# Optimization experiments

Hardware: AMD Instinct MI355X
Metric: run time of the kernel (lower is better)

The kernel has to match this reference:

```python
import jax, jax.numpy as jnp
from jax import lax
import numpy as np

EPS = 4e-3            # geoopt float32 ball boundary eps
MAXNORM = 1.0 - EPS   # c = 1 Poincare ball


def _norm(x):
    return jnp.sqrt(jnp.maximum(jnp.sum(x * x, axis=-1, keepdims=True), 1e-15))


def expmap0(u):
    n = _norm(u)
    return jnp.tanh(n) * u / n


def projx(x):
    n = _norm(x)
    return jnp.where(n > MAXNORM, x * (MAXNORM / n), x)


def mobius_add(x, y):
    x2 = jnp.sum(x * x, -1, keepdims=True)
    y2 = jnp.sum(y * y, -1, keepdims=True)
    xy = jnp.sum(x * y, -1, keepdims=True)
    num = (1.0 + 2.0 * xy + y2) * x + (1.0 - x2) * y
    den = 1.0 + 2.0 * xy + x2 * y2
    return num / jnp.maximum(den, 1e-15)


def mamba_layer(x, inW, convW, convb, xpW, dtW, dtb, A_log, Dp, outW):
    # x: [B,T,H]; inW: [2*Din,H]; convW: [Din,K]; xpW: [R+2N,Din]; dtW: [Din,R]
    B, T, H = x.shape
    Din, N = A_log.shape
    K = convW.shape[-1]
    R = dtW.shape[-1]
    xz = jnp.einsum('bth,dh->btd', x, inW)              # [B,T,2*Din]
    xr, z = jnp.split(xz, 2, axis=-1)
    xc = lax.conv_general_dilated(jnp.transpose(xr, (0, 2, 1)), convW[:, None, :],
                                  (1,), [(K - 1, 0)], feature_group_count=Din)
    u = jax.nn.silu(jnp.transpose(xc + convb[None, :, None], (0, 2, 1)))  # [B,T,Din]
    x_dbl = jnp.einsum('btd,ed->bte', u, xpW)           # [B,T,R+2N]
    dt_r, Bm, Cm = x_dbl[..., :R], x_dbl[..., R:R + N], x_dbl[..., R + N:]
    dt = jax.nn.softplus(jnp.einsum('btr,dr->btd', dt_r, dtW) + dtb)      # [B,T,Din]
    A = -jnp.exp(A_log)                                 # [Din,N]
    dA = jnp.exp(dt[..., None] * A)                     # [B,T,Din,N]
    dBu = dt[..., None] * Bm[:, :, None, :] * u[..., None]

    def step(h, ins):
        dA_t, dBu_t, C_t = ins
        h = dA_t * h + dBu_t                            # [B,Din,N]
        return h, jnp.einsum('bdn,bn->bd', h, C_t)

    h0 = jnp.zeros((B, Din, N), x.dtype)
    _, ys = lax.scan(step, h0, (jnp.moveaxis(dA, 1, 0), jnp.moveaxis(dBu, 1, 0), jnp.moveaxis(Cm, 1, 0)))
    y = jnp.moveaxis(ys, 0, 1) + Dp * u                 # [B,T,Din]
    return jnp.einsum('btd,hd->bth', y * jax.nn.silu(z), outW)


def _encode(xs, inp_W, inp_b, in_proj_W, conv_W, conv_b, xproj_W, dt_W, dt_b, A_log, D_skip, out_W, outp_W, outp_b):
    # xs: [4,B,T,1]; params carry leading branch dim 4, then layer dim 3
    def branch(x, iW, ib, ipW, cW, cb, xpW, dW, db, Al, Dp, oW, opW, opb):
        h = jnp.einsum('bti,hi->bth', x, iW) + ib
        for l in range(ipW.shape[0]):
            h = mamba_layer(h, ipW[l], cW[l], cb[l], xpW[l], dW[l], db[l], Al[l], Dp[l], oW[l])
        return jnp.tanh(jnp.einsum('bth,eh->bte', h, opW) + opb)
    return jax.vmap(branch)(xs, inp_W, inp_b, in_proj_W, conv_W, conv_b, xproj_W, dt_W, dt_b, A_log, D_skip, out_W, outp_W, outp_b)


def setup_inputs() -> dict:
    key = jax.random.key(0)
    ks = jax.random.split(key, 24)
    Br, B, T, H, Din, N, K, R, E, L = 4, 32, 1024, 64, 128, 16, 4, 4, 32, 3

    def rn(k, shape, s=0.05):
        return jax.random.normal(k, shape, jnp.float32) * s

    A_init = jnp.log(jnp.arange(1, N + 1, dtype=jnp.float32))
    return {
        'trend': jax.random.normal(ks[0], (B, T, 1), jnp.float32),
        'seasonal_weekly': jax.random.normal(ks[1], (B, T, 1), jnp.float32),
        'seasonal_daily': jax.random.normal(ks[2], (B, T, 1), jnp.float32),
        'residual': jax.random.normal(ks[3], (B, T, 1), jnp.float32),
        'inp_W': rn(ks[4], (Br, H, 1), 0.5),
        'inp_b': rn(ks[5], (Br, H)),
        'in_proj_W': rn(ks[6], (Br, L, 2 * Din, H)),
        'conv_W': rn(ks[7], (Br, L, Din, K), 0.2),
        'conv_b': rn(ks[8], (Br, L, Din)),
        'xproj_W': rn(ks[9], (Br, L, R + 2 * N, Din)),
        'dt_W': rn(ks[10], (Br, L, Din, R), 0.2),
        'dt_b': rn(ks[11], (Br, L, Din), 0.5) - 4.0,  # softplus(dt_b) small
        'A_log': jnp.tile(A_init, (Br, L, Din, 1)) + rn(ks[12], (Br, L, Din, N), 0.01),
        'D_skip': jnp.ones((Br, L, Din), jnp.float32) + rn(ks[13], (Br, L, Din), 0.01),
        'out_W': rn(ks[14], (Br, L, H, Din)),
        'outp_W': rn(ks[15], (Br, E, H)),
        'outp_b': rn(ks[16], (Br, E)),
    }


def reference(trend, seasonal_weekly, seasonal_daily, residual, inp_W, inp_b, in_proj_W, conv_W, conv_b, xproj_W, dt_W, dt_b, A_log, D_skip, out_W, outp_W, outp_b):
    xs = jnp.stack([trend, seasonal_weekly, seasonal_daily, residual], 0)  # [4,B,T,1]
    z = _encode(xs, inp_W, inp_b, in_proj_W, conv_W, conv_b, xproj_W, dt_W, dt_b, A_log, D_skip, out_W, outp_W, outp_b)  # [4,B,T,E]
    zh = projx(expmap0(z))
    t, w, d, r = zh[0], zh[1], zh[2], zh[3]
    comb = projx(mobius_add(mobius_add(t, mobius_add(w, d)), r))
    # stacked [trend_h, weekly_h, daily_h, residual_h, combined_h]
    return jnp.stack([t, w, d, r, comb], 0)
```

## Files before the change

kernel.cpp:

```cpp
#include <hip/hip_runtime.h>
#include <math.h>

#define TT 1024
#define DIN 128
#define HH 64
#define NN 16
#define EE 32
#define LL 3
#define BB 32

__device__ __forceinline__ float siluf(float x) { return x / (1.f + __expf(-x)); }

typedef __attribute__((ext_vector_type(8))) short bf16x8;
typedef __attribute__((ext_vector_type(4))) float f32x4;

__device__ __forceinline__ void split2(float x, ushort& hi, ushort& lo) {
  unsigned u = __float_as_uint(x);
  hi = (ushort)(u >> 16);
  float rem = x - __uint_as_float((u >> 16) << 16);
  lo = (ushort)(__float_as_uint(rem) >> 16);
}

#define WXZ_N 196608
#define WXD_N 73728
#define WOUT_N 98304

__global__ __launch_bounds__(256) void k_presplit(
    const float* __restrict__ iprojW, const float* __restrict__ xprojW,
    const float* __restrict__ outW,
    ushort* __restrict__ WxzH, ushort* __restrict__ WxzL,
    ushort* __restrict__ WxdH, ushort* __restrict__ WxdL,
    ushort* __restrict__ WoH, ushort* __restrict__ WoL) {
  int idx = blockIdx.x * 256 + threadIdx.x;
  if (idx < WXZ_N) {
    ushort h, l;
    split2(iprojW[idx], h, l);
    WxzH[idx] = h; WxzL[idx] = l;
  }
  if (idx < WXD_N) {
    int k = idx & 127, r = (idx >> 7) % 48, bl = idx / (48 * 128);
    float v = (r < 36) ? xprojW[((size_t)(bl * 36 + r)) * 128 + k] : 0.f;
    ushort h, l;
    split2(v, h, l);
    WxdH[idx] = h; WxdL[idx] = l;
  }
  if (idx < WOUT_N) {
    ushort h, l;
    split2(outW[idx], h, l);
    WoH[idx] = h; WoL[idx] = l;
  }
}

__global__ __launch_bounds__(256) void k_xz(
    const float* __restrict__ x0, const float* __restrict__ x1,
    const float* __restrict__ x2, const float* __restrict__ x3,
    const float* __restrict__ h, const ushort* __restrict__ WH,
    const ushort* __restrict__ WL,
    const float* __restrict__ inpW, const float* __restrict__ inpb,
    float* __restrict__ xr, float* __restrict__ zb, int br0, int l) {
  __shared__ __align__(16) ushort Hh[64][72], Hl[64][72];
  const int tid = threadIdx.x;
  const int b  = blockIdx.y;
  const int t0 = blockIdx.x * 64;
  const int br = br0 + (b >> 5);
  const float* Hg = h + ((size_t)b * TT + t0) * HH;
  {
    const int row = tid >> 2, c0 = (tid & 3) * 16;
    float xv = 0.f;
    if (l == 0) {
      int bb = b & 31;
      const float* xp = (br == 0) ? x0 : (br == 1) ? x1 : (br == 2) ? x2 : x3;
      xv = xp[bb * TT + t0 + row];
    }
    #pragma unroll
    for (int q = 0; q < 4; ++q) {
      float4 hv;
      if (l == 0) {
        float4 w4 = *(const float4*)(inpW + br * HH + c0 + q * 4);
        float4 b4 = *(const float4*)(inpb + br * HH + c0 + q * 4);
        hv.x = xv * w4.x + b4.x; hv.y = xv * w4.y + b4.y;
        hv.z = xv * w4.z + b4.z; hv.w = xv * w4.w + b4.w;
      } else {
        hv = *(const float4*)(Hg + (size_t)row * HH + c0 + q * 4);
      }
      ushort h0,h1,h2,h3,l0,l1,l2,l3;
      split2(hv.x,h0,l0); split2(hv.y,h1,l1); split2(hv.z,h2,l2); split2(hv.w,h3,l3);
      *(ushort4*)&Hh[row][c0 + q*4] = make_ushort4(h0,h1,h2,h3);
      *(ushort4*)&Hl[row][c0 + q*4] = make_ushort4(l0,l1,l2,l3);
    }
  }
  __syncthreads();
  const int wave = tid >> 6, lane = tid & 63;
  const int quad = lane >> 4, l16 = lane & 15;
  const int nsub = (wave & 1) * 32, tsub = (wave >> 1) * 32;
  const size_t wbase = (size_t)(br * LL + l) * 256;
  for (int n0 = 0; n0 < 2 * DIN; n0 += 64) {
    f32x4 acc[2][2] = {};
    #pragma unroll
    for (int k0 = 0; k0 < 64; k0 += 32) {
      bf16x8 Ah[2], Al[2], Bh[2], Bl[2];
      #pragma unroll
      for (int i = 0; i < 2; ++i) {
        size_t ro = (wbase + n0 + nsub + i * 16 + l16) * 64 + k0 + quad * 8;
        Ah[i] = *(const bf16x8*)(WH + ro);
        Al[i] = *(const bf16x8*)(WL + ro);
        Bh[i] = *(const bf16x8*)&Hh[tsub + i*16 + l16][k0 + quad*8];
        Bl[i] = *(const bf16x8*)&Hl[tsub + i*16 + l16][k0 + quad*8];
      }
      #pragma unroll
      for (int i = 0; i < 2; ++i)
        #pragma unroll
        for (int j = 0; j < 2; ++j) {
          acc[i][j] = __builtin_amdgcn_mfma_f32_16x16x32_bf16(Ah[i], Bh[j], acc[i][j], 0, 0, 0);
          acc[i][j] = __builtin_amdgcn_mfma_f32_16x16x32_bf16(Ah[i], Bl[j], acc[i][j], 0, 0, 0);
          acc[i][j] = __builtin_amdgcn_mfma_f32_16x16x32_bf16(Al[i], Bh[j], acc[i][j], 0, 0, 0);
        }
    }
    #pragma unroll
    for (int i = 0; i < 2; ++i) {
      #pragma unroll
      for (int r = 0; r < 4; ++r) {
        int n = n0 + nsub + i*16 + quad*4 + r;
        float* dst = (n < DIN) ? (xr + ((size_t)b * DIN + n) * TT)
                               : (zb + ((size_t)b * DIN + (n - DIN)) * TT);
        #pragma unroll
        for (int j = 0; j < 2; ++j)
          dst[t0 + tsub + j*16 + l16] = acc[i][j][r];
      }
    }
  }
}

__global__ __launch_bounds__(256) void k_xds(
    const float* __restrict__ xr, const float* __restrict__ convW,
    const float* __restrict__ convb, const ushort* __restrict__ WH,
    const ushort* __restrict__ WL, const float* __restrict__ dtW,
    const float* __restrict__ dtb, const float* __restrict__ A_log,
    const float* __restrict__ D_skip,
    float* __restrict__ cd, float* __restrict__ Cm,
    float* __restrict__ Hloc, float* __restrict__ g, float* __restrict__ sdt,
    int br0, int l) {
  __shared__ __align__(16) float U[128][66];
  __shared__ __align__(16) float Xs[40][68];
  const int tid = threadIdx.x;
  const int b  = blockIdx.y;
  const int c  = blockIdx.x;
  const int t0 = c * 64;
  const int br = br0 + (b >> 5);
  const int wave = tid >> 6, lane = tid & 63;
  const int quad = lane >> 4, l16 = lane & 15;
  const int tw = wave * 16;
  const size_t wb48 = (size_t)(br * LL + l) * 48 * 128;
  const int dd = tid >> 1, p = tid & 1;
  {
    const int tb = t0 + p * 32;
    const float* src = xr + ((size_t)b * DIN + dd) * TT + tb;
    float r[36];
    #pragma unroll
    for (int q = 0; q < 9; ++q) {
      float4 f = make_float4(0.f, 0.f, 0.f, 0.f);
      if (q > 0 || tb > 0) f = *(const float4*)(src - 4 + q * 4);
      r[q*4+0] = f.x; r[q*4+1] = f.y; r[q*4+2] = f.z; r[q*4+3] = f.w;
    }
    const int wb0 = (br * LL + l) * DIN + dd;
    const float* w = convW + (size_t)wb0 * 4;
    const float w0 = w[0], w1 = w[1], w2 = w[2], w3 = w[3];
    const float cb = convb[wb0];
    #pragma unroll
    for (int i = 0; i < 32; i += 2) {
      float o0 = siluf(r[i+1]*w0 + r[i+2]*w1 + r[i+3]*w2 + r[i+4]*w3 + cb);
      float o1 = siluf(r[i+2]*w0 + r[i+3]*w1 + r[i+4]*w2 + r[i+5]*w3 + cb);
      *(float2*)&U[dd][p * 32 + i] = make_float2(o0, o1);
    }
  }
  __syncthreads();
  f32x4 acc[3] = {};
  #pragma unroll
  for (int k0 = 0; k0 < DIN; k0 += 32) {
    ushort bh[8], bl[8];
    #pragma unroll
    for (int j = 0; j < 8; ++j)
      split2(U[k0 + quad * 8 + j][tw + l16], bh[j], bl[j]);
    bf16x8 Bh = *(bf16x8*)bh, Bl = *(bf16x8*)bl;
    #pragma unroll
    for (int nf = 0; nf < 3; ++nf) {
      size_t ro = wb48 + (size_t)(nf * 16 + l16) * 128 + k0 + quad * 8;
      bf16x8 Whf = *(const bf16x8*)(WH + ro);
      bf16x8 Wlf = *(const bf16x8*)(WL + ro);
      acc[nf] = __builtin_amdgcn_mfma_f32_16x16x32_bf16(Whf, Bh, acc[nf], 0, 0, 0);
      acc[nf] = __builtin_amdgcn_mfma_f32_16x16x32_bf16(Whf, Bl, acc[nf], 0, 0, 0);
      acc[nf] = __builtin_amdgcn_mfma_f32_16x16x32_bf16(Wlf, Bh, acc[nf], 0, 0, 0);
    }
  }
  #pragma unroll
  for (int nf = 0; nf < 3; ++nf) {
    #pragma unroll
    for (int r = 0; r < 4; ++r) {
      int n = nf * 16 + quad * 4 + r;
      if (n < 40) Xs[n][tw + l16] = acc[nf][r];
    }
  }
  __syncthreads();
  {
    int n = tid >> 4, i0 = (tid & 15) * 4;
    *(float4*)(Cm + ((size_t)b * NN + n) * TT + t0 + i0) = *(float4*)&Xs[20 + n][i0];
  }
  const int n0s = p * 8;
  const int wbase = (br * LL + l) * DIN + dd;
  const float* wd = dtW + (size_t)wbase * 4;
  const float w0 = wd[0], w1 = wd[1], w2 = wd[2], w3 = wd[3];
  const float bias = dtb[wbase];
  float Ac[8];
  #pragma unroll
  for (int j = 0; j < 8; ++j) Ac[j] = -__expf(A_log[(size_t)wbase * NN + n0s + j]);
  const float Dp = D_skip[wbase];
  float hst[8] = {0.f,0.f,0.f,0.f,0.f,0.f,0.f,0.f};
  float sd = 0.f;
  float* gp  = g  + ((size_t)b * DIN + dd) * TT + t0;
  float* cdp = cd + ((size_t)b * DIN + dd) * TT + t0;
  for (int t8 = 0; t8 < 64; t8 += 8) {
    float4 a0 = *(const float4*)&Xs[0][t8], a0b = *(const float4*)&Xs[0][t8 + 4];
    float4 a1 = *(const float4*)&Xs[1][t8], a1b = *(const float4*)&Xs[1][t8 + 4];
    float4 a2 = *(const float4*)&Xs[2][t8], a2b = *(const float4*)&Xs[2][t8 + 4];
    float4 a3 = *(const float4*)&Xs[3][t8], a3b = *(const float4*)&Xs[3][t8 + 4];
    float x0v[8] = {a0.x,a0.y,a0.z,a0.w,a0b.x,a0b.y,a0b.z,a0b.w};
    float x1v[8] = {a1.x,a1.y,a1.z,a1.w,a1b.x,a1b.y,a1b.z,a1b.w};
    float x2v[8] = {a2.x,a2.y,a2.z,a2.w,a2b.x,a2b.y,a2b.z,a2b.w};
    float x3v[8] = {a3.x,a3.y,a3.z,a3.w,a3b.x,a3b.y,a3b.z,a3b.w};
    float us[8];
    {
      float2 u0 = *(const float2*)&U[dd][t8];
      float2 u1 = *(const float2*)&U[dd][t8 + 2];
      float2 u2 = *(const float2*)&U[dd][t8 + 4];
      float2 u3 = *(const float2*)&U[dd][t8 + 6];
      us[0]=u0.x; us[1]=u0.y; us[2]=u1.x; us[3]=u1.y;
      us[4]=u2.x; us[5]=u2.y; us[6]=u3.x; us[7]=u3.y;
    }
    float dts[8], cds[8], du[8];
    #pragma unroll
    for (int s = 0; s < 8; ++s) {
      float sv = x0v[s]*w0 + x1v[s]*w1 + x2v[s]*w2 + x3v[s]*w3 + bias;
      float e = __expf(-fabsf(sv));
      float dtv = fmaxf(sv, 0.f) + __logf(1.f + e);
      sd += dtv;
      dts[s] = dtv;
      cds[s] = sd;
      du[s] = dtv * us[s];
    }
    float acc8[8] = {0.f,0.f,0.f,0.f,0.f,0.f,0.f,0.f};
    #pragma unroll
    for (int j = 0; j < 8; ++j) {
      int n = n0s + j;
      float4 bq0 = *(const float4*)&Xs[4 + n][t8];
      float4 bq1 = *(const float4*)&Xs[4 + n][t8 + 4];
      float4 cq0 = *(const float4*)&Xs[20 + n][t8];
      float4 cq1 = *(const float4*)&Xs[20 + n][t8 + 4];
      float Bv[8] = {bq0.x,bq0.y,bq0.z,bq0.w,bq1.x,bq1.y,bq1.z,bq1.w};
      float Cv[8] = {cq0.x,cq0.y,cq0.z,cq0.w,cq1.x,cq1.y,cq1.z,cq1.w};
      float hj = hst[j], an = Ac[j];
      #pragma unroll
      for (int s = 0; s < 8; ++s) {
        hj = __expf(dts[s] * an) * hj + du[s] * Bv[s];
        acc8[s] += hj * Cv[s];
      }
      hst[j] = hj;
    }
    #pragma unroll
    for (int s = 0; s < 8; ++s) {
      float tot = acc8[s] + __shfl_xor(acc8[s], 1, 2);
      acc8[s] = tot + Dp * us[s];
    }
    if (p == 0) {
      *(float4*)(gp + t8)      = make_float4(acc8[0], acc8[1], acc8[2], acc8[3]);
      *(float4*)(gp + t8 + 4)  = make_float4(acc8[4], acc8[5], acc8[6], acc8[7]);
      *(float4*)(cdp + t8)     = make_float4(cds[0], cds[1], cds[2], cds[3]);
      *(float4*)(cdp + t8 + 4) = make_float4(cds[4], cds[5], cds[6], cds[7]);
    }
  }
  {
    float* hp = Hloc + (((size_t)b * DIN + dd) * 16 + c) * 16 + n0s;
    *(float4*)hp       = make_float4(hst[0], hst[1], hst[2], hst[3]);
    *(float4*)(hp + 4) = make_float4(hst[4], hst[5], hst[6], hst[7]);
  }
  if (p == 0) sdt[((size_t)b * DIN + dd) * 16 + c] = sd;
}

__global__ __launch_bounds__(256) void k_scan2(
    const float* __restrict__ cdc, const float* __restrict__ Cm,
    const float* __restrict__ A_log, const float* __restrict__ Hloc,
    const float* __restrict__ sdt, float* __restrict__ g, int br0, int l) {
  __shared__ __align__(16) float Cl[16][68];
  __shared__ __align__(16) float HinL[32][16];
  const int bx  = blockIdx.x;
  const int b   = bx / 60;
  const int rem = bx % 60;
  const int c   = (rem >> 2) + 1;
  const int dq  = rem & 3;
  const int tid = threadIdx.x;
  const int br  = br0 + (b >> 5);
  {
    int row = tid >> 4, cc = (tid & 15) * 4;
    *(float4*)&Cl[row][cc] = *(const float4*)(Cm + ((size_t)b * NN + row) * TT + c * 64 + cc);
  }
  const int dloc = tid >> 3, tg = tid & 7;
  const int d  = dq * 32 + dloc;
  size_t off = ((size_t)b * DIN + d) * TT + c * 64 + tg * 8;
  float* gp = g + off;
  float4 y0 = *(const float4*)gp;
  float4 y1 = *(const float4*)(gp + 4);
  float4 cq0 = *(const float4*)(cdc + off);
  float4 cq1 = *(const float4*)(cdc + off + 4);
  {
    int n0 = (tid & 7) * 2;
    int wbase = (br * LL + l) * DIN + d;
    float a0 = -__expf(A_log[(size_t)wbase * NN + n0]);
    float a1 = -__expf(A_log[(size_t)wbase * NN + n0 + 1]);
    float h0 = 0.f, h1 = 0.f;
    const float* sp  = sdt + ((size_t)b * DIN + d) * 16;
    const float* hlb = Hloc + ((size_t)b * DIN + d) * 256;
    for (int cc = 0; cc < c; ++cc) {
      float sdv = sp[cc];
      float2 hl = *(const float2*)(hlb + cc * 16 + n0);
      h0 = __expf(a0 * sdv) * h0 + hl.x;
      h1 = __expf(a1 * sdv) * h1 + hl.y;
    }
    HinL[dloc][n0] = h0;
    HinL[dloc][n0 + 1] = h1;
  }
  __syncthreads();
  float cd8[8] = {cq0.x, cq0.y, cq0.z, cq0.w, cq1.x, cq1.y, cq1.z, cq1.w};
  const float* al = A_log + (size_t)((br * LL + l) * DIN + d) * NN;
  float Ac16[16];
  #pragma unroll
  for (int n = 0; n < 16; ++n) Ac16[n] = -__expf(al[n]);
  float y8[8] = {y0.x, y0.y, y0.z, y0.w, y1.x, y1.y, y1.z, y1.w};
  const int tbase = tg * 8;
  #pragma unroll
  for (int n = 0; n < 16; ++n) {
    float hv = HinL[dloc][n];
    float an = Ac16[n];
    #pragma unroll
    for (int s = 0; s < 8; ++s)
      y8[s] += Cl[n][tbase + s] * __expf(an * cd8[s]) * hv;
  }
  *(float4*)gp       = make_float4(y8[0], y8[1], y8[2], y8[3]);
  *(float4*)(gp + 4) = make_float4(y8[4], y8[5], y8[6], y8[7]);
}

__global__ __launch_bounds__(256) void k_outxz(
    const float* __restrict__ graw, float* zb,
    const ushort* __restrict__ WoHp, const ushort* __restrict__ WoLp,
    const ushort* __restrict__ WxHp, const ushort* __restrict__ WxLp,
    float* __restrict__ xr, int br0, int l) {
  __shared__ __align__(16) ushort Bh_[64][72], Bl_[64][72];
  const int tid = threadIdx.x;
  const int b  = blockIdx.y;
  const int t0 = blockIdx.x * 64;
  const int br = br0 + (b >> 5);
  const int wave = tid >> 6, lane = tid & 63;
  const int quad = lane >> 4, l16 = lane & 15;
  const int hsub = (wave & 1) * 32, tsub = (wave >> 1) * 32;
  const size_t wbo = (size_t)(br * LL + l) * 64;
  f32x4 acc[2][2] = {};
  for (int k0 = 0; k0 < DIN; k0 += 64) {
    __syncthreads();
    {
      int row = tid >> 2, c0 = (tid & 3) * 16;
      #pragma unroll
      for (int q = 0; q < 4; ++q) {
        size_t off = ((size_t)b * DIN + k0 + row) * TT + t0 + c0 + q * 4;
        float4 gv = *(const float4*)(graw + off);
        float4 zv = *(const float4*)(zb + off);
        float a0 = gv.x * siluf(zv.x), a1 = gv.y * siluf(zv.y);
        float a2 = gv.z * siluf(zv.z), a3 = gv.w * siluf(zv.w);
        ushort h0,h1,h2,h3,l0,l1,l2,l3;
        split2(a0,h0,l0); split2(a1,h1,l1); split2(a2,h2,l2); split2(a3,h3,l3);
        *(ushort4*)&Bh_[row][c0 + q*4] = make_ushort4(h0,h1,h2,h3);
        *(ushort4*)&Bl_[row][c0 + q*4] = make_ushort4(l0,l1,l2,l3);
      }
    }
    __syncthreads();
    #pragma unroll
    for (int kk = 0; kk < 64; kk += 32) {
      bf16x8 Ahf[2], Alf[2], Bhf[2], Blf[2];
      #pragma unroll
      for (int i = 0; i < 2; ++i) {
        size_t ro = (wbo + hsub + i * 16 + l16) * 128 + k0 + kk + quad * 8;
        Ahf[i] = *(const bf16x8*)(WoHp + ro);
        Alf[i] = *(const bf16x8*)(WoLp + ro);
        Bhf[i] = *(const bf16x8*)&Bh_[tsub + i*16 + l16][kk + quad*8];
        Blf[i] = *(const bf16x8*)&Bl_[tsub + i*16 + l16][kk + quad*8];
      }
      #pragma unroll
      for (int i = 0; i < 2; ++i)
        #pragma unroll
        for (int j = 0; j < 2; ++j) {
          acc[i][j] = __builtin_amdgcn_mfma_f32_16x16x32_bf16(Ahf[i], Bhf[j], acc[i][j], 0, 0, 0);
          acc[i][j] = __builtin_amdgcn_mfma_f32_16x16x32_bf16(Ahf[i], Blf[j], acc[i][j], 0, 0, 0);
          acc[i][j] = __builtin_amdgcn_mfma_f32_16x16x32_bf16(Alf[i], Bhf[j], acc[i][j], 0, 0, 0);
        }
    }
  }
  __syncthreads();
  #pragma unroll
  for (int i = 0; i < 2; ++i) {
    int hh0 = hsub + i*16 + quad*4;
    #pragma unroll
    for (int j = 0; j < 2; ++j) {
      int t = tsub + j*16 + l16;
      ushort h0,h1,h2,h3,l0,l1,l2,l3;
      split2(acc[i][j][0],h0,l0); split2(acc[i][j][1],h1,l1);
      split2(acc[i][j][2],h2,l2); split2(acc[i][j][3],h3,l3);
      *(ushort2*)&Bh_[t][hh0]     = make_ushort2(h0,h1);
      *(ushort2*)&Bh_[t][hh0 + 2] = make_ushort2(h2,h3);
      *(ushort2*)&Bl_[t][hh0]     = make_ushort2(l0,l1);
      *(ushort2*)&Bl_[t][hh0 + 2] = make_ushort2(l2,l3);
    }
  }
  __syncthreads();
  const size_t wbase = (size_t)(br * LL + (l + 1)) * 256;
  const int nsub = hsub;
  for (int n0 = 0; n0 < 2 * DIN; n0 += 64) {
    f32x4 a2[2][2] = {};
    #pragma unroll
    for (int k0 = 0; k0 < 64; k0 += 32) {
      bf16x8 Ah[2], Al[2], Bh[2], Bl[2];
      #pragma unroll
      for (int i = 0; i < 2; ++i) {
        size_t ro = (wbase + n0 + nsub + i * 16 + l16) * 64 + k0 + quad * 8;
        Ah[i] = *(const bf16x8*)(WxHp + ro);
        Al[i] = *(const bf16x8*)(WxLp + ro);
        Bh[i] = *(const bf16x8*)&Bh_[tsub + i*16 + l16][k0 + quad*8];
        Bl[i] = *(const bf16x8*)&Bl_[tsub + i*16 + l16][k0 + quad*8];
      }
      #pragma unroll
      for (int i = 0; i < 2; ++i)
        #pragma unroll
        for (int j = 0; j < 2; ++j) {
          a2[i][j] = __builtin_amdgcn_mfma_f32_16x16x32_bf16(Ah[i], Bh[j], a2[i][j], 0, 0, 0);
          a2[i][j] = __builtin_amdgcn_mfma_f32_16x16x32_bf16(Ah[i], Bl[j], a2[i][j], 0, 0, 0);
          a2[i][j] = __builtin_amdgcn_mfma_f32_16x16x32_bf16(Al[i], Bh[j], a2[i][j], 0, 0, 0);
        }
    }
    #pragma unroll
    for (int i = 0; i < 2; ++i) {
      #pragma unroll
      for (int r = 0; r < 4; ++r) {
        int n = n0 + nsub + i*16 + quad*4 + r;
        float* dst = (n < DIN) ? (xr + ((size_t)b * DIN + n) * TT)
                               : (zb + ((size_t)b * DIN + (n - DIN)) * TT);
        #pragma unroll
        for (int j = 0; j < 2; ++j)
          dst[t0 + tsub + j*16 + l16] = a2[i][j][r];
      }
    }
  }
}

__global__ __launch_bounds__(256) void k_out(
    const float* __restrict__ graw, const float* __restrict__ zb,
    const ushort* __restrict__ WH, const ushort* __restrict__ WL,
    float* __restrict__ h, int br0, int l) {
  __shared__ __align__(16) ushort Bh_[64][72], Bl_[64][72];
  const int tid = threadIdx.x;
  const int b  = blockIdx.y;
  const int t0 = blockIdx.x * 64;
  const int br = br0 + (b >> 5);
  const int wave = tid >> 6, lane = tid & 63;
  const int quad = lane >> 4, l16 = lane & 15;
  const int hsub = (wave & 1) * 32, tsub = (wave >> 1) * 32;
  const size_t wb = (size_t)(br * LL + l) * 64;
  f32x4 acc[2][2] = {};
  for (int k0 = 0; k0 < DIN; k0 += 64) {
    __syncthreads();
    {
      int row = tid >> 2, c0 = (tid & 3) * 16;
      #pragma unroll
      for (int q = 0; q < 4; ++q) {
        size_t off = ((size_t)b * DIN + k0 + row) * TT + t0 + c0 + q * 4;
        float4 gv = *(const float4*)(graw + off);
        float4 zv = *(const float4*)(zb + off);
        float a0 = gv.x * siluf(zv.x), a1 = gv.y * siluf(zv.y);
        float a2 = gv.z * siluf(zv.z), a3 = gv.w * siluf(zv.w);
        ushort h0,h1,h2,h3,l0,l1,l2,l3;
        split2(a0,h0,l0); split2(a1,h1,l1); split2(a2,h2,l2); split2(a3,h3,l3);
        *(ushort4*)&Bh_[row][c0 + q*4] = make_ushort4(h0,h1,h2,h3);
        *(ushort4*)&Bl_[row][c0 + q*4] = make_ushort4(l0,l1,l2,l3);
      }
    }
    __syncthreads();
    #pragma unroll
    for (int kk = 0; kk < 64; kk += 32) {
      bf16x8 Ahf[2], Alf[2], Bhf[2], Blf[2];
      #pragma unroll
      for (int i = 0; i < 2; ++i) {
        size_t ro = (wb + hsub + i * 16 + l16) * 128 + k0 + kk + quad * 8;
        Ahf[i] = *(const bf16x8*)(WH + ro);
        Alf[i] = *(const bf16x8*)(WL + ro);
        Bhf[i] = *(const bf16x8*)&Bh_[tsub + i*16 + l16][kk + quad*8];
        Blf[i] = *(const bf16x8*)&Bl_[tsub + i*16 + l16][kk + quad*8];
      }
      #pragma unroll
      for (int i = 0; i < 2; ++i)
        #pragma unroll
        for (int j = 0; j < 2; ++j) {
          acc[i][j] = __builtin_amdgcn_mfma_f32_16x16x32_bf16(Ahf[i], Bhf[j], acc[i][j], 0, 0, 0);
          acc[i][j] = __builtin_amdgcn_mfma_f32_16x16x32_bf16(Ahf[i], Blf[j], acc[i][j], 0, 0, 0);
          acc[i][j] = __builtin_amdgcn_mfma_f32_16x16x32_bf16(Alf[i], Bhf[j], acc[i][j], 0, 0, 0);
        }
    }
  }
  #pragma unroll
  for (int i = 0; i < 2; ++i) {
    int hh0 = hsub + i*16 + quad*4;
    #pragma unroll
    for (int j = 0; j < 2; ++j) {
      int t = t0 + tsub + j*16 + l16;
      *(f32x4*)(h + ((size_t)b * TT + t) * HH + hh0) = acc[i][j];
    }
  }
}

__global__ __launch_bounds__(256) void k_ze(
    const float* __restrict__ h, const float* __restrict__ outpW,
    const float* __restrict__ outpb, float* __restrict__ ze, int br0) {
  __shared__ __align__(16) float As[16][132];
  __shared__ __align__(16) float Ws[16][36];
  __shared__ __align__(16) float Cs[128][36];
  const int tid = threadIdx.x;
  const int b  = blockIdx.y;
  const int t0 = blockIdx.x * 128;
  const int br = br0 + (b >> 5);
  const float* W = outpW + (size_t)br * EE * HH;
  float acc[4][4] = {};
  const int ti = tid & 31, ni = tid >> 5;
  for (int k0 = 0; k0 < HH; k0 += 16) {
    __syncthreads();
    {
      int i = tid >> 1, kq = (tid & 1) * 8;
      const float* src = h + ((size_t)b * TT + t0 + i) * HH + k0 + kq;
      float4 a0 = *(const float4*)src;
      float4 a1 = *(const float4*)(src + 4);
      As[kq+0][i]=a0.x; As[kq+1][i]=a0.y; As[kq+2][i]=a0.z; As[kq+3][i]=a0.w;
      As[kq+4][i]=a1.x; As[kq+5][i]=a1.y; As[kq+6][i]=a1.z; As[kq+7][i]=a1.w;
    }
    for (int idx = tid; idx < 512; idx += 256) {
      int jj = idx >> 4, kk = idx & 15;
      Ws[kk][jj] = W[(size_t)jj * HH + k0 + kk];
    }
    __syncthreads();
    #pragma unroll
    for (int kk = 0; kk < 16; ++kk) {
      float4 a = *(const float4*)&As[kk][ti * 4];
      float4 w = *(const float4*)&Ws[kk][ni * 4];
      acc[0][0] += a.x*w.x; acc[0][1] += a.x*w.y; acc[0][2] += a.x*w.z; acc[0][3] += a.x*w.w;
      acc[1][0] += a.y*w.x; acc[1][1] += a.y*w.y; acc[1][2] += a.y*w.z; acc[1][3] += a.y*w.w;
      acc[2][0] += a.z*w.x; acc[2][1] += a.z*w.y; acc[2][2] += a.z*w.z; acc[2][3] += a.z*w.w;
      acc[3][0] += a.w*w.x; acc[3][1] += a.w*w.y; acc[3][2] += a.w*w.z; acc[3][3] += a.w*w.w;
    }
  }
  __syncthreads();
  float bj[4];
  #pragma unroll
  for (int c = 0; c < 4; ++c) bj[c] = outpb[br * EE + ni*4 + c];
  #pragma unroll
  for (int r = 0; r < 4; ++r)
    #pragma unroll
    for (int c = 0; c < 4; ++c)
      Cs[ti*4+r][ni*4+c] = tanhf(acc[r][c] + bj[c]);
  __syncthreads();
  int i = tid >> 1, j16 = (tid & 1) * 16;
  float* dst = ze + (((size_t)(br0 * 32 + b)) * TT + t0 + i) * EE + j16;
  #pragma unroll
  for (int q = 0; q < 4; ++q)
    *(float4*)(dst + q*4) = *(float4*)&Cs[i][j16 + q*4];
}

__device__ __forceinline__ void mobius_add32(const float* x, const float* y, float* o) {
  float x2 = 0.f, y2 = 0.f, xy = 0.f;
  #pragma unroll
  for (int i = 0; i < 32; ++i) { x2 += x[i]*x[i]; y2 += y[i]*y[i]; xy += x[i]*y[i]; }
  float ca  = 1.f + 2.f*xy + y2;
  float cb  = 1.f - x2;
  float den = 1.f + 2.f*xy + x2*y2;
  float inv = 1.f / fmaxf(den, 1e-15f);
  #pragma unroll
  for (int i = 0; i < 32; ++i) o[i] = (ca*x[i] + cb*y[i]) * inv;
}

__global__ __launch_bounds__(256) void k_hyper(const float* __restrict__ ze,
                                               float* __restrict__ out) {
  int idx = blockIdx.x * 256 + threadIdx.x;
  int b = idx >> 10, t = idx & 1023;
  float v[4][32];
  #pragma unroll
  for (int br = 0; br < 4; ++br) {
    const float* p = ze + (((size_t)br * BB + b) * TT + t) * EE;
    float s = 0.f;
    #pragma unroll
    for (int e = 0; e < 32; ++e) { v[br][e] = p[e]; s += v[br][e]*v[br][e]; }
    float nr = sqrtf(fmaxf(s, 1e-15f));
    float sc = tanhf(nr) / nr;
    float s2 = 0.f;
    #pragma unroll
    for (int e = 0; e < 32; ++e) { v[br][e] *= sc; s2 += v[br][e]*v[br][e]; }
    float n2 = sqrtf(fmaxf(s2, 1e-15f));
    if (n2 > 0.996f) {
      float sc2 = 0.996f / n2;
      #pragma unroll
      for (int e = 0; e < 32; ++e) v[br][e] *= sc2;
    }
    float* o = out + (((size_t)br * BB + b) * TT + t) * EE;
    #pragma unroll
    for (int e = 0; e < 32; ++e) o[e] = v[br][e];
  }
  float m1[32], m2[32];
  mobius_add32(v[1], v[2], m1);
  mobius_add32(v[0], m1, m2);
  mobius_add32(m2, v[3], m1);
  float s = 0.f;
  #pragma unroll
  for (int e = 0; e < 32; ++e) s += m1[e]*m1[e];
  float n = sqrtf(fmaxf(s, 1e-15f));
  if (n > 0.996f) {
    float sc = 0.996f / n;
    #pragma unroll
    for (int e = 0; e < 32; ++e) m1[e] *= sc;
  }
  float* o = out + (((size_t)4 * BB + b) * TT + t) * EE;
  #pragma unroll
  for (int e = 0; e < 32; ++e) o[e] = m1[e];
}

extern "C" void kernel_launch(void* const* d_in, const int* in_sizes, int n_in,
                              void* d_out, int out_size, void* d_ws, size_t ws_size,
                              hipStream_t stream) {
  const float* xs0 = (const float*)d_in[0];
  const float* xs1 = (const float*)d_in[1];
  const float* xs2 = (const float*)d_in[2];
  const float* xs3 = (const float*)d_in[3];
  const float* inpW   = (const float*)d_in[4];
  const float* inpb   = (const float*)d_in[5];
  const float* iprojW = (const float*)d_in[6];
  const float* convW  = (const float*)d_in[7];
  const float* convb  = (const float*)d_in[8];
  const float* xprojW = (const float*)d_in[9];
  const float* dtW    = (const float*)d_in[10];
  const float* dtb    = (const float*)d_in[11];
  const float* A_log  = (const float*)d_in[12];
  const float* D_skip = (const float*)d_in[13];
  const float* outW   = (const float*)d_in[14];
  const float* outpW  = (const float*)d_in[15];
  const float* outpb  = (const float*)d_in[16];
  float* out = (float*)d_out;

  const size_t wUshorts = 2 * (WXZ_N + WXD_N + WOUT_N);
  ushort* WxzH = (ushort*)d_ws;
  ushort* WxzL = WxzH + WXZ_N;
  ushort* WxdH = WxzL + WXZ_N;
  ushort* WxdL = WxdH + WXD_N;
  ushort* WoH  = WxdL + WXD_N;
  ushort* WoL  = WoH + WOUT_N;
  float* ws = (float*)(WoL + WOUT_N);

  const size_t zeF = (size_t)4 * BB * TT * EE;
  const size_t perBl = 65536 + 4 * 131072 + 2 * 16384 + 2048;
  auto needBytes = [&](int NB) {
    return (zeF + (size_t)NB * 32 * perBl) * 4 + wUshorts * 2;
  };
  int NB = 4;
  if (needBytes(4) > ws_size) NB = 2;
  if (NB == 2 && needBytes(2) > ws_size) NB = 1;
  const int nbl = NB * 32;

  float* ze = ws;
  float* h  = ze + zeF;
  float* xr = h  + (size_t)nbl * 65536;
  float* zb = xr + (size_t)nbl * 131072;
  float* g  = zb + (size_t)nbl * 131072;
  float* cd = g  + (size_t)nbl * 131072;
  float* Bm = cd + (size_t)nbl * 131072;
  float* Cm = Bm + (size_t)nbl * 16384;
  float* sdt = Cm + (size_t)nbl * 16384;
  float* Hloc = h;
  (void)Bm;

  k_presplit<<<WXZ_N / 256, 256, 0, stream>>>(iprojW, xprojW, outW,
                                              WxzH, WxzL, WxdH, WxdL, WoH, WoL);

  for (int br0 = 0; br0 < 4; br0 += NB) {
    for (int l = 0; l < LL; ++l) {
      if (l == 0)
        k_xz<<<dim3(16, nbl), 256, 0, stream>>>(xs0, xs1, xs2, xs3, h,
                                                WxzH, WxzL, inpW, inpb, xr, zb, br0, 0);
      k_xds  <<<dim3(16, nbl), 256, 0, stream>>>(xr, convW, convb, WxdH, WxdL,
                                                 dtW, dtb, A_log, D_skip,
                                                 cd, Cm, Hloc, g, sdt, br0, l);
      k_scan2<<<nbl * 60, 256, 0, stream>>>(cd, Cm, A_log, Hloc, sdt, g, br0, l);
      if (l < LL - 1)
        k_outxz<<<dim3(16, nbl), 256, 0, stream>>>(g, zb, WoH, WoL, WxzH, WxzL,
                                                   xr, br0, l);
      else
        k_out<<<dim3(16, nbl), 256, 0, stream>>>(g, zb, WoH, WoL, h, br0, l);
    }
    k_ze<<<dim3(8, nbl), 256, 0, stream>>>(h, outpW, outpb, ze, br0);
  }
  k_hyper<<<BB * TT / 256, 256, 0, stream>>>(ze, out);
}
```

Baseline: 965.1 us.

## Fuse chunk-scan correction into output projection kernels and split dt softplus across thread pairs

Removes the separate k_scan2 kernel by folding the inter-chunk state propagation and carry-in correction into k_outxz/k_out, which now compute incoming states per chunk and add the C·exp(A·cumdt)·h term before the output GEMM. k_xds now computes the dt softplus for only half the timesteps per thread and exchanges the rest via a shuffle, and shrinks the Xs buffer. k_xz is specialised to layer 0 only, and Hloc gets its own workspace buffer instead of aliasing h. This saves a launch and a full read/write of g per layer, but adds heavy per-element exp work (16 exps per output) inside the GEMM staging loop and uneven load across chunk blocks.

```diff
diff --git a/kernel.cpp b/kernel.cpp
--- a/kernel.cpp
+++ b/kernel.cpp
@@ -54,35 +54,26 @@
 __global__ __launch_bounds__(256) void k_xz(
     const float* __restrict__ x0, const float* __restrict__ x1,
     const float* __restrict__ x2, const float* __restrict__ x3,
-    const float* __restrict__ h, const ushort* __restrict__ WH,
-    const ushort* __restrict__ WL,
+    const ushort* __restrict__ WH, const ushort* __restrict__ WL,
     const float* __restrict__ inpW, const float* __restrict__ inpb,
-    float* __restrict__ xr, float* __restrict__ zb, int br0, int l) {
+    float* __restrict__ xr, float* __restrict__ zb, int br0) {
   __shared__ __align__(16) ushort Hh[64][72], Hl[64][72];
   const int tid = threadIdx.x;
   const int b  = blockIdx.y;
   const int t0 = blockIdx.x * 64;
   const int br = br0 + (b >> 5);
-  const float* Hg = h + ((size_t)b * TT + t0) * HH;
   {
     const int row = tid >> 2, c0 = (tid & 3) * 16;
-    float xv = 0.f;
-    if (l == 0) {
-      int bb = b & 31;
-      const float* xp = (br == 0) ? x0 : (br == 1) ? x1 : (br == 2) ? x2 : x3;
-      xv = xp[bb * TT + t0 + row];
-    }
+    int bb = b & 31;
+    const float* xp = (br == 0) ? x0 : (br == 1) ? x1 : (br == 2) ? x2 : x3;
+    float xv = xp[bb * TT + t0 + row];
     #pragma unroll
     for (int q = 0; q < 4; ++q) {
+      float4 w4 = *(const float4*)(inpW + br * HH + c0 + q * 4);
+      float4 b4 = *(const float4*)(inpb + br * HH + c0 + q * 4);
       float4 hv;
-      if (l == 0) {
-        float4 w4 = *(const float4*)(inpW + br * HH + c0 + q * 4);
-        float4 b4 = *(const float4*)(inpb + br * HH + c0 + q * 4);
-        hv.x = xv * w4.x + b4.x; hv.y = xv * w4.y + b4.y;
-        hv.z = xv * w4.z + b4.z; hv.w = xv * w4.w + b4.w;
-      } else {
-        hv = *(const float4*)(Hg + (size_t)row * HH + c0 + q * 4);
-      }
+      hv.x = xv * w4.x + b4.x; hv.y = xv * w4.y + b4.y;
+      hv.z = xv * w4.z + b4.z; hv.w = xv * w4.w + b4.w;
       ushort h0,h1,h2,h3,l0,l1,l2,l3;
       split2(hv.x,h0,l0); split2(hv.y,h1,l1); split2(hv.z,h2,l2); split2(hv.w,h3,l3);
       *(ushort4*)&Hh[row][c0 + q*4] = make_ushort4(h0,h1,h2,h3);
@@ -93,7 +84,7 @@
   const int wave = tid >> 6, lane = tid & 63;
   const int quad = lane >> 4, l16 = lane & 15;
   const int nsub = (wave & 1) * 32, tsub = (wave >> 1) * 32;
-  const size_t wbase = (size_t)(br * LL + l) * 256;
+  const size_t wbase = (size_t)(br * LL) * 256;
   for (int n0 = 0; n0 < 2 * DIN; n0 += 64) {
     f32x4 acc[2][2] = {};
     #pragma unroll
@@ -141,7 +132,7 @@
     float* __restrict__ Hloc, float* __restrict__ g, float* __restrict__ sdt,
     int br0, int l) {
   __shared__ __align__(16) float U[128][66];
-  __shared__ __align__(16) float Xs[40][68];
+  __shared__ __align__(16) float Xs[36][68];
   const int tid = threadIdx.x;
   const int b  = blockIdx.y;
   const int c  = blockIdx.x;
@@ -197,7 +188,7 @@
     #pragma unroll
     for (int r = 0; r < 4; ++r) {
       int n = nf * 16 + quad * 4 + r;
-      if (n < 40) Xs[n][tw + l16] = acc[nf][r];
+      if (n < 36) Xs[n][tw + l16] = acc[nf][r];
     }
   }
   __syncthreads();
@@ -218,15 +209,32 @@
   float sd = 0.f;
   float* gp  = g  + ((size_t)b * DIN + dd) * TT + t0;
   float* cdp = cd + ((size_t)b * DIN + dd) * TT + t0;
+  const int sB = p * 4;
   for (int t8 = 0; t8 < 64; t8 += 8) {
-    float4 a0 = *(const float4*)&Xs[0][t8], a0b = *(const float4*)&Xs[0][t8 + 4];
-    float4 a1 = *(const float4*)&Xs[1][t8], a1b = *(const float4*)&Xs[1][t8 + 4];
-    float4 a2 = *(const float4*)&Xs[2][t8], a2b = *(const float4*)&Xs[2][t8 + 4];
-    float4 a3 = *(const float4*)&Xs[3][t8], a3b = *(const float4*)&Xs[3][t8 + 4];
-    float x0v[8] = {a0.x,a0.y,a0.z,a0.w,a0b.x,a0b.y,a0b.z,a0b.w};
-    float x1v[8] = {a1.x,a1.y,a1.z,a1.w,a1b.x,a1b.y,a1b.z,a1b.w};
-    float x2v[8] = {a2.x,a2.y,a2.z,a2.w,a2b.x,a2b.y,a2b.z,a2b.w};
-    float x3v[8] = {a3.x,a3.y,a3.z,a3.w,a3b.x,a3b.y,a3b.z,a3b.w};
+    float4 aa0 = *(const float4*)&Xs[0][t8 + sB];
+    float4 aa1 = *(const float4*)&Xs[1][t8 + sB];
+    float4 aa2 = *(const float4*)&Xs[2][t8 + sB];
+    float4 aa3 = *(const float4*)&Xs[3][t8 + sB];
+    float x0a[4] = {aa0.x, aa0.y, aa0.z, aa0.w};
+    float x1a[4] = {aa1.x, aa1.y, aa1.z, aa1.w};
+    float x2a[4] = {aa2.x, aa2.y, aa2.z, aa2.w};
+    float x3a[4] = {aa3.x, aa3.y, aa3.z, aa3.w};
+    float my[4];
+    #pragma unroll
+    for (int i = 0; i < 4; ++i) {
+      float sv = x0a[i]*w0 + x1a[i]*w1 + x2a[i]*w2 + x3a[i]*w3 + bias;
+      float e = __expf(-fabsf(sv));
+      my[i] = fmaxf(sv, 0.f) + __logf(1.f + e);
+    }
+    float ot[4];
+    #pragma unroll
+    for (int i = 0; i < 4; ++i) ot[i] = __shfl_xor(my[i], 1, 2);
+    float dts[8];
+    #pragma unroll
+    for (int i = 0; i < 4; ++i) {
+      dts[i]     = p ? ot[i] : my[i];
+      dts[4 + i] = p ? my[i] : ot[i];
+    }
     float us[8];
     {
       float2 u0 = *(const float2*)&U[dd][t8];
@@ -236,16 +244,12 @@
       us[0]=u0.x; us[1]=u0.y; us[2]=u1.x; us[3]=u1.y;
       us[4]=u2.x; us[5]=u2.y; us[6]=u3.x; us[7]=u3.y;
     }
-    float dts[8], cds[8], du[8];
+    float cds[8], du[8];
     #pragma unroll
     for (int s = 0; s < 8; ++s) {
-      float sv = x0v[s]*w0 + x1v[s]*w1 + x2v[s]*w2 + x3v[s]*w3 + bias;
-      float e = __expf(-fabsf(sv));
-      float dtv = fmaxf(sv, 0.f) + __logf(1.f + e);
-      sd += dtv;
-      dts[s] = dtv;
+      sd += dts[s];
       cds[s] = sd;
-      du[s] = dtv * us[s];
+      du[s] = dts[s] * us[s];
     }
     float acc8[8] = {0.f,0.f,0.f,0.f,0.f,0.f,0.f,0.f};
     #pragma unroll
@@ -285,98 +289,98 @@
   if (p == 0) sdt[((size_t)b * DIN + dd) * 16 + c] = sd;
 }
 
-__global__ __launch_bounds__(256) void k_scan2(
-    const float* __restrict__ cdc, const float* __restrict__ Cm,
-    const float* __restrict__ A_log, const float* __restrict__ Hloc,
-    const float* __restrict__ sdt, float* __restrict__ g, int br0, int l) {
-  __shared__ __align__(16) float Cl[16][68];
-  __shared__ __align__(16) float HinL[32][16];
-  const int bx  = blockIdx.x;
-  const int b   = bx / 60;
-  const int rem = bx % 60;
-  const int c   = (rem >> 2) + 1;
-  const int dq  = rem & 3;
-  const int tid = threadIdx.x;
-  const int br  = br0 + (b >> 5);
-  {
-    int row = tid >> 4, cc = (tid & 15) * 4;
-    *(float4*)&Cl[row][cc] = *(const float4*)(Cm + ((size_t)b * NN + row) * TT + c * 64 + cc);
-  }
-  const int dloc = tid >> 3, tg = tid & 7;
-  const int d  = dq * 32 + dloc;
-  size_t off = ((size_t)b * DIN + d) * TT + c * 64 + tg * 8;
-  float* gp = g + off;
-  float4 y0 = *(const float4*)gp;
-  float4 y1 = *(const float4*)(gp + 4);
-  float4 cq0 = *(const float4*)(cdc + off);
-  float4 cq1 = *(const float4*)(cdc + off + 4);
-  {
-    int n0 = (tid & 7) * 2;
-    int wbase = (br * LL + l) * DIN + d;
-    float a0 = -__expf(A_log[(size_t)wbase * NN + n0]);
-    float a1 = -__expf(A_log[(size_t)wbase * NN + n0 + 1]);
-    float h0 = 0.f, h1 = 0.f;
-    const float* sp  = sdt + ((size_t)b * DIN + d) * 16;
-    const float* hlb = Hloc + ((size_t)b * DIN + d) * 256;
-    for (int cc = 0; cc < c; ++cc) {
-      float sdv = sp[cc];
-      float2 hl = *(const float2*)(hlb + cc * 16 + n0);
-      h0 = __expf(a0 * sdv) * h0 + hl.x;
-      h1 = __expf(a1 * sdv) * h1 + hl.y;
-    }
-    HinL[dloc][n0] = h0;
-    HinL[dloc][n0 + 1] = h1;
-  }
-  __syncthreads();
-  float cd8[8] = {cq0.x, cq0.y, cq0.z, cq0.w, cq1.x, cq1.y, cq1.z, cq1.w};
-  const float* al = A_log + (size_t)((br * LL + l) * DIN + d) * NN;
-  float Ac16[16];
-  #pragma unroll
-  for (int n = 0; n < 16; ++n) Ac16[n] = -__expf(al[n]);
-  float y8[8] = {y0.x, y0.y, y0.z, y0.w, y1.x, y1.y, y1.z, y1.w};
-  const int tbase = tg * 8;
-  #pragma unroll
-  for (int n = 0; n < 16; ++n) {
-    float hv = HinL[dloc][n];
-    float an = Ac16[n];
-    #pragma unroll
-    for (int s = 0; s < 8; ++s)
-      y8[s] += Cl[n][tbase + s] * __expf(an * cd8[s]) * hv;
-  }
-  *(float4*)gp       = make_float4(y8[0], y8[1], y8[2], y8[3]);
-  *(float4*)(gp + 4) = make_float4(y8[4], y8[5], y8[6], y8[7]);
-}
-
 __global__ __launch_bounds__(256) void k_outxz(
     const float* __restrict__ graw, float* zb,
     const ushort* __restrict__ WoHp, const ushort* __restrict__ WoLp,
     const ushort* __restrict__ WxHp, const ushort* __restrict__ WxLp,
+    const float* __restrict__ cdc, const float* __restrict__ Cm,
+    const float* __restrict__ A_log, const float* __restrict__ Hloc,
+    const float* __restrict__ sdt,
     float* __restrict__ xr, int br0, int l) {
   __shared__ __align__(16) ushort Bh_[64][72], Bl_[64][72];
+  __shared__ __align__(16) float CmL[16][68];
+  __shared__ __align__(16) float HinL[128][17];
   const int tid = threadIdx.x;
   const int b  = blockIdx.y;
-  const int t0 = blockIdx.x * 64;
+  const int cb = blockIdx.x;
+  const int t0 = cb * 64;
   const int br = br0 + (b >> 5);
   const int wave = tid >> 6, lane = tid & 63;
   const int quad = lane >> 4, l16 = lane & 15;
   const int hsub = (wave & 1) * 32, tsub = (wave >> 1) * 32;
   const size_t wbo = (size_t)(br * LL + l) * 64;
+  if (cb > 0) {
+    const int ddh = tid >> 1, n0h = (tid & 1) * 8;
+    const size_t wbh = (size_t)((br * LL + l) * DIN + ddh) * NN + n0h;
+    float a8[8], h8[8];
+    #pragma unroll
+    for (int j = 0; j < 8; ++j) { a8[j] = -__expf(A_log[wbh + j]); h8[j] = 0.f; }
+    const float* sp  = sdt + ((size_t)b * DIN + ddh) * 16;
+    const float* hlb = Hloc + ((size_t)b * DIN + ddh) * 256 + n0h;
+    for (int cc = 0; cc < cb; ++cc) {
+      float sdv = sp[cc];
+      float4 hl0 = *(const float4*)(hlb + cc * 16);
+      float4 hl1 = *(const float4*)(hlb + cc * 16 + 4);
+      h8[0] = __expf(a8[0]*sdv)*h8[0] + hl0.x;
+      h8[1] = __expf(a8[1]*sdv)*h8[1] + hl0.y;
+      h8[2] = __expf(a8[2]*sdv)*h8[2] + hl0.z;
+      h8[3] = __expf(a8[3]*sdv)*h8[3] + hl0.w;
+      h8[4] = __expf(a8[4]*sdv)*h8[4] + hl1.x;
+      h8[5] = __expf(a8[5]*sdv)*h8[5] + hl1.y;
+      h8[6] = __expf(a8[6]*sdv)*h8[6] + hl1.z;
+      h8[7] = __expf(a8[7]*sdv)*h8[7] + hl1.w;
+    }
+    #pragma unroll
+    for (int j = 0; j < 8; ++j) HinL[ddh][n0h + j] = h8[j];
+    int rown = tid >> 4, ccl = (tid & 15) * 4;
+    *(float4*)&CmL[rown][ccl] = *(const float4*)(Cm + ((size_t)b * NN + rown) * TT + t0 + ccl);
+  }
   f32x4 acc[2][2] = {};
   for (int k0 = 0; k0 < DIN; k0 += 64) {
     __syncthreads();
     {
       int row = tid >> 2, c0 = (tid & 3) * 16;
-      #pragma unroll
-      for (int q = 0; q < 4; ++q) {
-        size_t off = ((size_t)b * DIN + k0 + row) * TT + t0 + c0 + q * 4;
-        float4 gv = *(const float4*)(graw + off);
-        float4 zv = *(const float4*)(zb + off);
-        float a0 = gv.x * siluf(zv.x), a1 = gv.y * siluf(zv.y);
-        float a2 = gv.z * siluf(zv.z), a3 = gv.w * siluf(zv.w);
-        ushort h0,h1,h2,h3,l0,l1,l2,l3;
-        split2(a0,h0,l0); split2(a1,h1,l1); split2(a2,h2,l2); split2(a3,h3,l3);
-        *(ushort4*)&Bh_[row][c0 + q*4] = make_ushort4(h0,h1,h2,h3);
-        *(ushort4*)&Bl_[row][c0 + q*4] = make_ushort4(l0,l1,l2,l3);
+      int d = k0 + row;
+      if (cb > 0) {
+        float Ac16[16], Hin16[16];
+        const float* al = A_log + (size_t)((br * LL + l) * DIN + d) * NN;
+        #pragma unroll
+        for (int n = 0; n < 16; ++n) { Ac16[n] = -__expf(al[n]); Hin16[n] = HinL[d][n]; }
+        #pragma unroll
+        for (int q = 0; q < 4; ++q) {
+          size_t off = ((size_t)b * DIN + d) * TT + t0 + c0 + q * 4;
+          float4 gv = *(const float4*)(graw + off);
+          float4 zv = *(const float4*)(zb + off);
+          float4 cdv = *(const float4*)(cdc + off);
+          int tq = c0 + q * 4;
+          #pragma unroll
+          for (int n = 0; n < 16; ++n) {
+            float hv = Hin16[n], an = Ac16[n];
+            gv.x += CmL[n][tq + 0] * __expf(an * cdv.x) * hv;
+            gv.y += CmL[n][tq + 1] * __expf(an * cdv.y) * hv;
+            gv.z += CmL[n][tq + 2] * __expf(an * cdv.z) * hv;
+            gv.w += CmL[n][tq + 3] * __expf(an * cdv.w) * hv;
+          }
+          float a0 = gv.x * siluf(zv.x), a1 = gv.y * siluf(zv.y);
+          float a2 = gv.z * siluf(zv.z), a3 = gv.w * siluf(zv.w);
+          ushort h0,h1,h2,h3,l0,l1,l2,l3;
+          split2(a0,h0,l0); split2(a1,h1,l1); split2(a2,h2,l2); split2(a3,h3,l3);
+          *(ushort4*)&Bh_[row][c0 + q*4] = make_ushort4(h0,h1,h2,h3);
+          *(ushort4*)&Bl_[row][c0 + q*4] = make_ushort4(l0,l1,l2,l3);
+        }
+      } else {
+        #pragma unroll
+        for (int q = 0; q < 4; ++q) {
+          size_t off = ((size_t)b * DIN + d) * TT + t0 + c0 + q * 4;
+          float4 gv = *(const float4*)(graw + off);
+          float4 zv = *(const float4*)(zb + off);
+          float a0 = gv.x * siluf(zv.x), a1 = gv.y * siluf(zv.y);
+          float a2 = gv.z * siluf(zv.z), a3 = gv.w * siluf(zv.w);
+          ushort h0,h1,h2,h3,l0,l1,l2,l3;
+          split2(a0,h0,l0); split2(a1,h1,l1); split2(a2,h2,l2); split2(a3,h3,l3);
+          *(ushort4*)&Bh_[row][c0 + q*4] = make_ushort4(h0,h1,h2,h3);
+          *(ushort4*)&Bl_[row][c0 + q*4] = make_ushort4(l0,l1,l2,l3);
+        }
       }
     }
     __syncthreads();
@@ -460,32 +464,94 @@
 __global__ __launch_bounds__(256) void k_out(
     const float* __restrict__ graw, const float* __restrict__ zb,
     const ushort* __restrict__ WH, const ushort* __restrict__ WL,
+    const float* __restrict__ cdc, const float* __restrict__ Cm,
+    const float* __restrict__ A_log, const float* __restrict__ Hloc,
+    const float* __restrict__ sdt,
     float* __restrict__ h, int br0, int l) {
   __shared__ __align__(16) ushort Bh_[64][72], Bl_[64][72];
+  __shared__ __align__(16) float CmL[16][68];
+  __shared__ __align__(16) float HinL[128][17];
   const int tid = threadIdx.x;
   const int b  = blockIdx.y;
-  const int t0 = blockIdx.x * 64;
+  const int cb = blockIdx.x;
+  const int t0 = cb * 64;
   const int br = br0 + (b >> 5);
   const int wave = tid >> 6, lane = tid & 63;
   const int quad = lane >> 4, l16 = lane & 15;
   const int hsub = (wave & 1) * 32, tsub = (wave >> 1) * 32;
   const size_t wb = (size_t)(br * LL + l) * 64;
+  if (cb > 0) {
+    const int ddh = tid >> 1, n0h = (tid & 1) * 8;
+    const size_t wbh = (size_t)((br * LL + l) * DIN + ddh) * NN + n0h;
+    float a8[8], h8[8];
+    #pragma unroll
+    for (int j = 0; j < 8; ++j) { a8[j] = -__expf(A_log[wbh + j]); h8[j] = 0.f; }
+    const float* sp  = sdt + ((size_t)b * DIN + ddh) * 16;
+    const float* hlb = Hloc + ((size_t)b * DIN + ddh) * 256 + n0h;
+    for (int cc = 0; cc < cb; ++cc) {
+      float sdv = sp[cc];
+      float4 hl0 = *(const float4*)(hlb + cc * 16);
+      float4 hl1 = *(const float4*)(hlb + cc * 16 + 4);
+      h8[0] = __expf(a8[0]*sdv)*h8[0] + hl0.x;
+      h8[1] = __expf(a8[1]*sdv)*h8[1] + hl0.y;
+      h8[2] = __expf(a8[2]*sdv)*h8[2] + hl0.z;
+      h8[3] = __expf(a8[3]*sdv)*h8[3] + hl0.w;
+      h8[4] = __expf(a8[4]*sdv)*h8[4] + hl1.x;
+      h8[5] = __expf(a8[5]*sdv)*h8[5] + hl1.y;
+      h8[6] = __expf(a8[6]*sdv)*h8[6] + hl1.z;
+      h8[7] = __expf(a8[7]*sdv)*h8[7] + hl1.w;
+    }
+    #pragma unroll
+    for (int j = 0; j < 8; ++j) HinL[ddh][n0h + j] = h8[j];
+    int rown = tid >> 4, ccl = (tid & 15) * 4;
+    *(float4*)&CmL[rown][ccl] = *(const float4*)(Cm + ((size_t)b * NN + rown) * TT + t0 + ccl);
+  }
   f32x4 acc[2][2] = {};
   for (int k0 = 0; k0 < DIN; k0 += 64) {
     __syncthreads();
     {
       int row = tid >> 2, c0 = (tid & 3) * 16;
-      #pragma unroll
-      for (int q = 0; q < 4; ++q) {
-        size_t off = ((size_t)b * DIN + k0 + row) * TT + t0 + c0 + q * 4;
-        float4 gv = *(const float4*)(graw + off);
-        float4 zv = *(const float4*)(zb + off);
-        float a0 = gv.x * siluf(zv.x), a1 = gv.y * siluf(zv.y);
-        float a2 = gv.z * siluf(zv.z), a3 = gv.w * siluf(zv.w);
-        ushort h0,h1,h2,h3,l0,l1,l2,l3;
-        split2(a0,h0,l0); split2(a1,h1,l1); split2(a2,h2,l2); split2(a3,h3,l3);
-        *(ushort4*)&Bh_[row][c0 + q*4] = make_ushort4(h0,h1,h2,h3);
-        *(ushort4*)&Bl_[row][c0 + q*4] = make_ushort4(l0,l1,l2,l3);
+      int d = k0 + row;
+      if (cb > 0) {
+        float Ac16[16], Hin16[16];
+        const float* al = A_log + (size_t)((br * LL + l) * DIN + d) * NN;
+        #pragma unroll
+        for (int n = 0; n < 16; ++n) { Ac16[n] = -__expf(al[n]); Hin16[n] = HinL[d][n]; }
+        #pragma unroll
+        for (int q = 0; q < 4; ++q) {
+          size_t off = ((size_t)b * DIN + d) * TT + t0 + c0 + q * 4;
+          float4 gv = *(const float4*)(graw + off);
+          float4 zv = *(const float4*)(zb + off);
+          float4 cdv = *(const float4*)(cdc + off);
+          int tq = c0 + q * 4;
+          #pragma unroll
+          for (int n = 0; n < 16; ++n) {
+            float hv = Hin16[n], an = Ac16[n];
+            gv.x += CmL[n][tq + 0] * __expf(an * cdv.x) * hv;
+            gv.y += CmL[n][tq + 1] * __expf(an * cdv.y) * hv;
+            gv.z += CmL[n][tq + 2] * __expf(an * cdv.z) * hv;
+            gv.w += CmL[n][tq + 3] * __expf(an * cdv.w) * hv;
+          }
+          float a0 = gv.x * siluf(zv.x), a1 = gv.y * siluf(zv.y);
+          float a2 = gv.z * siluf(zv.z), a3 = gv.w * siluf(zv.w);
+          ushort h0,h1,h2,h3,l0,l1,l2,l3;
+          split2(a0,h0,l0); split2(a1,h1,l1); split2(a2,h2,l2); split2(a3,h3,l3);
+          *(ushort4*)&Bh_[row][c0 + q*4] = make_ushort4(h0,h1,h2,h3);
+          *(ushort4*)&Bl_[row][c0 + q*4] = make_ushort4(l0,l1,l2,l3);
+        }
+      } else {
+        #pragma unroll
+        for (int q = 0; q < 4; ++q) {
+          size_t off = ((size_t)b * DIN + d) * TT + t0 + c0 + q * 4;
+          float4 gv = *(const float4*)(graw + off);
+          float4 zv = *(const float4*)(zb + off);
+          float a0 = gv.x * siluf(zv.x), a1 = gv.y * siluf(zv.y);
+          float a2 = gv.z * siluf(zv.z), a3 = gv.w * siluf(zv.w);
+          ushort h0,h1,h2,h3,l0,l1,l2,l3;
+          split2(a0,h0,l0); split2(a1,h1,l1); split2(a2,h2,l2); split2(a3,h3,l3);
+          *(ushort4*)&Bh_[row][c0 + q*4] = make_ushort4(h0,h1,h2,h3);
+          *(ushort4*)&Bl_[row][c0 + q*4] = make_ushort4(l0,l1,l2,l3);
+        }
       }
     }
     __syncthreads();
@@ -664,7 +730,7 @@
   float* ws = (float*)(WoL + WOUT_N);
 
   const size_t zeF = (size_t)4 * BB * TT * EE;
-  const size_t perBl = 65536 + 4 * 131072 + 2 * 16384 + 2048;
+  const size_t perBl = 65536 + 4 * 131072 + 32768 + 16384 + 2048;
   auto needBytes = [&](int NB) {
     return (zeF + (size_t)NB * 32 * perBl) * 4 + wUshorts * 2;
   };
@@ -679,29 +745,28 @@
   float* zb = xr + (size_t)nbl * 131072;
   float* g  = zb + (size_t)nbl * 131072;
   float* cd = g  + (size_t)nbl * 131072;
-  float* Bm = cd + (size_t)nbl * 131072;
-  float* Cm = Bm + (size_t)nbl * 16384;
+  float* Hloc = cd + (size_t)nbl * 131072;
+  float* Cm = Hloc + (size_t)nbl * 32768;
   float* sdt = Cm + (size_t)nbl * 16384;
-  float* Hloc = h;
-  (void)Bm;
 
   k_presplit<<<WXZ_N / 256, 256, 0, stream>>>(iprojW, xprojW, outW,
                                               WxzH, WxzL, WxdH, WxdL, WoH, WoL);
 
   for (int br0 = 0; br0 < 4; br0 += NB) {
+    k_xz<<<dim3(16, nbl), 256, 0, stream>>>(xs0, xs1, xs2, xs3,
+                                            WxzH, WxzL, inpW, inpb, xr, zb, br0);
     for (int l = 0; l < LL; ++l) {
-      if (l == 0)
-        k_xz<<<dim3(16, nbl), 256, 0, stream>>>(xs0, xs1, xs2, xs3, h,
-                                                WxzH, WxzL, inpW, inpb, xr, zb, br0, 0);
-      k_xds  <<<dim3(16, nbl), 256, 0, stream>>>(xr, convW, convb, WxdH, WxdL,
-                                                 dtW, dtb, A_log, D_skip,
-                                                 cd, Cm, Hloc, g, sdt, br0, l);
-      k_scan2<<<nbl * 60, 256, 0, stream>>>(cd, Cm, A_log, Hloc, sdt, g, br0, l);
+      k_xds<<<dim3(16, nbl), 256, 0, stream>>>(xr, convW, convb, WxdH, WxdL,
+                                               dtW, dtb, A_log, D_skip,
+                                               cd, Cm, Hloc, g, sdt, br0, l);
       if (l < LL - 1)
         k_outxz<<<dim3(16, nbl), 256, 0, stream>>>(g, zb, WoH, WoL, WxzH, WxzL,
+                                                   cd, Cm, A_log, Hloc, sdt,
                                                    xr, br0, l);
       else
-        k_out<<<dim3(16, nbl), 256, 0, stream>>>(g, zb, WoH, WoL, h, br0, l);
+        k_out<<<dim3(16, nbl), 256, 0, stream>>>(g, zb, WoH, WoL,
+                                                 cd, Cm, A_log, Hloc, sdt,
+                                                 h, br0, l);
     }
     k_ze<<<dim3(8, nbl), 256, 0, stream>>>(h, outpW, outpb, ze, br0);
   }
```

Measured after the change: 1.033 ms. 7.0% more time.
